# Kernel tuning notes

Measured on AMD Instinct MI355X. Metric: run time of the kernel, lower is better.

## Reference

```python
import jax, jax.numpy as jnp
import numpy as np

N, E, NF, EF, F = 50000, 100000, 20000, 40000, 10000
CIN, C, ED, S, H, L = 128, 128, 16, 8, 8, 3
EPS = 1e-5


def setup_inputs() -> dict:
    key = jax.random.key(0)
    ks = jax.random.split(key, 20)
    p = lambda k, shp: jax.random.normal(k, shp, dtype=jnp.float32) * 0.05
    return {
        "x": jax.random.normal(ks[0], (N, CIN), dtype=jnp.float32),
        "edge_attr": jax.random.normal(ks[1], (E, ED), dtype=jnp.float32),
        "frag_x": jax.random.normal(ks[2], (NF, CIN), dtype=jnp.float32),
        "frag_edge_attr": jax.random.normal(ks[3], (EF, ED), dtype=jnp.float32),
        "la_w": p(ks[4], (CIN, C)), "la_b": jnp.zeros((C,), jnp.float32),
        "lb_w": p(ks[5], (ED, C)), "lb_b": jnp.zeros((C,), jnp.float32),
        "bn1_g": jnp.ones((C,), jnp.float32), "bn1_b": jnp.zeros((C,), jnp.float32),
        "bn2_g": jnp.ones((C,), jnp.float32), "bn2_b": jnp.zeros((C,), jnp.float32),
        "wn": p(ks[6], (L, C, C)),
        "wb": p(ks[7], (L, S, C, C)),
        "wl": p(ks[8], (L, 3 * C, S)),
        "wlb": jnp.zeros((L, S), jnp.float32),
        "gate_w": p(ks[9], (3 * C, C)), "gate_b": jnp.zeros((C,), jnp.float32),
        "gat_wsrc": p(ks[10], (C, H * C)), "gat_wdst": p(ks[11], (C, H * C)),
        "gat_asrc": p(ks[12], (H, C)), "gat_adst": p(ks[13], (H, C)),
        "gat_bias": jnp.zeros((C,), jnp.float32),
        "out_w": p(ks[14], (2 * C, 1)), "out_b": jnp.zeros((1,), jnp.float32),
        "edge_index": jax.random.randint(ks[15], (2, E), 0, N),
        "frag_edge_index": jax.random.randint(ks[16], (2, EF), 0, NF),
        # sorted, covers every cluster id in [0, F) (each appears NF//F times)
        "cluster_index": (jnp.arange(NF) * F) // NF,
        "num_clusters": F,
    }


def reference(x, edge_attr, frag_x, frag_edge_attr, la_w, la_b, lb_w, lb_b,
              bn1_g, bn1_b, bn2_g, bn2_b, wn, wb, wl, wlb, gate_w, gate_b,
              gat_wsrc, gat_wdst, gat_asrc, gat_adst, gat_bias, out_w, out_b,
              edge_index, frag_edge_index, cluster_index, num_clusters):
    def bn(z, g, b):  # training-mode batch norm (biased var)
        mu = jnp.mean(z, 0)
        var = jnp.mean((z - mu) ** 2, 0)
        return (z - mu) * jax.lax.rsqrt(var + EPS) * g + b

    def ntn(h, ei, ea, Wn, Wb, Wl, bl):
        n = h.shape[0]
        xp = h @ Wn            # [n, C] node projection
        ep = ea @ Wn           # [e, C] (module reuses weight_node for edges)
        src, dst = ei[0], ei[1]
        xi, xj = xp[dst], xp[src]                       # per-edge gathers
        score = jnp.einsum('ec,scd,ed->es', xi, Wb, xj)  # bilinear score [e,S]
        block = jnp.concatenate([xi, ep, xj], axis=1) @ Wl + bl  # [e,S]
        alpha = jnp.tanh(score + block)
        e = xi.shape[0]
        msg = (jnp.maximum(xj, ep).reshape(e, S, C // S) * alpha[:, :, None]).reshape(e, C)
        return jax.ops.segment_sum(msg, dst, num_segments=n)  # aggr='add'

    def stack(h, ei, ea):
        for l in range(L):
            hh = jax.nn.relu(ntn(h, ei, ea, wn[l], wb[l], wl[l], wlb[l]))
            beta = jax.nn.relu(jnp.concatenate([h, hh, h - hh], axis=1) @ gate_w + gate_b)
            h = beta * h + (1.0 - beta) * hh
        return h

    # atom path
    x1 = jax.nn.relu(bn(x @ la_w + la_b, bn1_g, bn1_b))
    ea1 = jax.nn.relu(bn(edge_attr @ lb_w + lb_b, bn2_g, bn2_b))
    x1 = stack(x1, edge_index, ea1)
    mol_vec = jax.nn.relu(x1)  # global_add_pool with batch=arange(N) is identity

    # fragment path
    fx = jax.nn.relu(frag_x @ la_w + la_b)
    fea = jax.nn.relu(bn(frag_edge_attr @ lb_w + lb_b, bn2_g, bn2_b))
    fx = stack(fx, frag_edge_index, fea)
    frag_pool = jax.nn.relu(jax.ops.segment_sum(fx, cluster_index, num_segments=num_clusters))
    # consecutive_cluster perm = first occurrence of each cluster id (cluster_index sorted)
    perm = jnp.searchsorted(cluster_index, jnp.arange(num_clusters))

    # GATConv cross-attention, bipartite (frag_pool -> mol_vec), heads averaged
    n = mol_vec.shape[0]
    h_src = (frag_pool @ gat_wsrc).reshape(num_clusters, H, C)
    h_dst = (mol_vec @ gat_wdst).reshape(n, H, C)
    a_src = jnp.sum(h_src * gat_asrc, -1)   # [F,H]
    a_dst = jnp.sum(h_dst * gat_adst, -1)   # [n,H]
    el = jax.nn.leaky_relu(a_src + a_dst[perm], 0.01)
    m = jax.ops.segment_max(el, perm, num_segments=n)
    ex = jnp.exp(el - m[perm])
    sden = jax.ops.segment_sum(ex, perm, num_segments=n)
    att = ex / sden[perm]
    agg = jax.ops.segment_sum(h_src * att[:, :, None], perm, num_segments=n)
    frag_m_vec = jax.nn.relu(jnp.mean(agg, 1) + gat_bias)

    return jnp.concatenate([mol_vec, frag_m_vec], axis=1) @ out_w + out_b
```

## Files before the change

kernel.cpp:

```cpp
#include <hip/hip_runtime.h>
#include <hip/hip_bf16.h>
#include <hip/hip_fp8.h>

#define EPS 1e-5f

typedef short bf16x8 __attribute__((ext_vector_type(8)));
typedef short short4v __attribute__((ext_vector_type(4)));
typedef short short16v __attribute__((ext_vector_type(16)));
typedef float f32x4 __attribute__((ext_vector_type(4)));
typedef float f32x2 __attribute__((ext_vector_type(2)));
typedef unsigned char uchar16v __attribute__((ext_vector_type(16)));

static __device__ __forceinline__ short f2bf(float x) {
    __hip_bfloat16 h = __float2bfloat16(x);
    return *reinterpret_cast<short*>(&h);
}
static __device__ __forceinline__ float bf2f(short x) {
    __hip_bfloat16 h;
    *reinterpret_cast<short*>(&h) = x;
    return __bfloat162float(h);
}
static __device__ __forceinline__ unsigned char f2fp8(float x) {
    __hip_fp8_e4m3 q(x);
    return (unsigned char)q.__x;
}
static __device__ __forceinline__ float fp82f(unsigned char b) {
    __hip_fp8_e4m3 q;
    q.__x = (__hip_fp8_storage_t)b;
    return (float)q;
}
static __device__ __forceinline__ unsigned pack4_fp8(float v0, float v1, float v2, float v3) {
#if __has_builtin(__builtin_amdgcn_cvt_pk_fp8_f32)
    int pk = __builtin_amdgcn_cvt_pk_fp8_f32(v0, v1, 0, false);
    pk = __builtin_amdgcn_cvt_pk_fp8_f32(v2, v3, pk, true);
    return (unsigned)pk;
#else
    return (unsigned)f2fp8(v0) | ((unsigned)f2fp8(v1) << 8) |
           ((unsigned)f2fp8(v2) << 16) | ((unsigned)f2fp8(v3) << 24);
#endif
}
template<bool HI>
static __device__ __forceinline__ f32x2 unpack2_fp8(int w) {
#if __has_builtin(__builtin_amdgcn_cvt_pk_f32_fp8)
    return __builtin_amdgcn_cvt_pk_f32_fp8(w, HI);
#else
    f32x2 r;
    const int sh = HI ? 16 : 0;
    r[0] = fp82f((unsigned char)((w >> sh) & 0xff));
    r[1] = fp82f((unsigned char)((w >> (sh + 8)) & 0xff));
    return r;
#endif
}

template<int SPLIT, int ACT, int OUTM>
__global__ __launch_bounds__(256) void gemm_split(const float* __restrict__ A,
                                                  const short* __restrict__ BTh,
                                                  const short* __restrict__ BTl,
                                                  const float* __restrict__ bias,
                                                  void* __restrict__ Cout,
                                                  void* __restrict__ Cout2,
                                                  int M, int N, int K) {
    __shared__ short Ah[128][40];
    __shared__ short Al[128][40];
    __shared__ short Bh[128][40];
    __shared__ short Bl[128][40];
    const int tid = threadIdx.x;
    const int row0 = blockIdx.y * 128, col0 = blockIdx.x * 128;
    const int lane = tid & 63, w = tid >> 6;
    const int wr = w >> 1, wc = w & 1;
    const int lr = lane & 15, lg = lane >> 4;
    f32x4 acc[4][4] = {};

    for (int k0 = 0; k0 < K; k0 += 32) {
        #pragma unroll
        for (int i = 0; i < 4; ++i) {
            int idx = i * 256 + tid;
            int r = idx >> 3, q = idx & 7;
            int gr = row0 + r, gk = k0 + q * 4;
            f32x4 v;
            if (gr < M && gk + 3 < K) {
                v = *reinterpret_cast<const f32x4*>(&A[(size_t)gr * K + gk]);
            } else {
                #pragma unroll
                for (int j = 0; j < 4; ++j)
                    v[j] = (gr < M && gk + j < K) ? A[(size_t)gr * K + gk + j] : 0.f;
            }
            short4v h, l;
            #pragma unroll
            for (int j = 0; j < 4; ++j) {
                h[j] = f2bf(v[j]);
                l[j] = f2bf(v[j] - bf2f(h[j]));
            }
            *reinterpret_cast<short4v*>(&Ah[r][q * 4]) = h;
            *reinterpret_cast<short4v*>(&Al[r][q * 4]) = l;
        }
        #pragma unroll
        for (int i = 0; i < 4; ++i) {
            int idx = i * 256 + tid;
            int r = idx >> 3, q = idx & 7;
            int gc = col0 + r, gk = k0 + q * 4;
            short4v u, ul;
            if (gk + 3 < K) {
                u = *reinterpret_cast<const short4v*>(&BTh[(size_t)gc * K + gk]);
                if (SPLIT == 3) ul = *reinterpret_cast<const short4v*>(&BTl[(size_t)gc * K + gk]);
            } else {
                #pragma unroll
                for (int j = 0; j < 4; ++j) {
                    u[j] = (gk + j < K) ? BTh[(size_t)gc * K + gk + j] : (short)0;
                    if (SPLIT == 3) ul[j] = (gk + j < K) ? BTl[(size_t)gc * K + gk + j] : (short)0;
                }
            }
            *reinterpret_cast<short4v*>(&Bh[r][q * 4]) = u;
            if (SPLIT == 3) *reinterpret_cast<short4v*>(&Bl[r][q * 4]) = ul;
        }
        __syncthreads();
        bf16x8 afh[4], afl[4], bfh[4];
        #pragma unroll
        for (int mi = 0; mi < 4; ++mi) {
            afh[mi] = *reinterpret_cast<const bf16x8*>(&Ah[wr * 64 + mi * 16 + lr][lg * 8]);
            afl[mi] = *reinterpret_cast<const bf16x8*>(&Al[wr * 64 + mi * 16 + lr][lg * 8]);
        }
        #pragma unroll
        for (int ni = 0; ni < 4; ++ni)
            bfh[ni] = *reinterpret_cast<const bf16x8*>(&Bh[wc * 64 + ni * 16 + lr][lg * 8]);
        #pragma unroll
        for (int mi = 0; mi < 4; ++mi)
            #pragma unroll
            for (int ni = 0; ni < 4; ++ni) {
                acc[mi][ni] = __builtin_amdgcn_mfma_f32_16x16x32_bf16(afh[mi], bfh[ni], acc[mi][ni], 0, 0, 0);
                acc[mi][ni] = __builtin_amdgcn_mfma_f32_16x16x32_bf16(afl[mi], bfh[ni], acc[mi][ni], 0, 0, 0);
            }
        if (SPLIT == 3) {
            bf16x8 bfl[4];
            #pragma unroll
            for (int ni = 0; ni < 4; ++ni)
                bfl[ni] = *reinterpret_cast<const bf16x8*>(&Bl[wc * 64 + ni * 16 + lr][lg * 8]);
            #pragma unroll
            for (int mi = 0; mi < 4; ++mi)
                #pragma unroll
                for (int ni = 0; ni < 4; ++ni)
                    acc[mi][ni] = __builtin_amdgcn_mfma_f32_16x16x32_bf16(afh[mi], bfl[ni], acc[mi][ni], 0, 0, 0);
        }
        __syncthreads();
    }

    #pragma unroll
    for (int mi = 0; mi < 4; ++mi) {
        #pragma unroll
        for (int ni = 0; ni < 4; ++ni) {
            int col = col0 + wc * 64 + ni * 16 + lr;
            float bv = bias ? bias[col] : 0.f;
            #pragma unroll
            for (int r = 0; r < 4; ++r) {
                int row = row0 + wr * 64 + mi * 16 + lg * 4 + r;
                if (row >= M) continue;
                float v = acc[mi][ni][r] + bv;
                if (ACT) v = fmaxf(v, 0.f);
                if (OUTM == 0) ((float*)Cout)[(size_t)row * N + col] = v;
                else ((short*)Cout)[(size_t)row * N + col] = f2bf(v);
            }
        }
    }
}

__global__ __launch_bounds__(256) void ep_gemm64(const short* __restrict__ A,
                                                 const short* __restrict__ BT,
                                                 short* __restrict__ Cout, int M) {
    __shared__ short Bf[128 * 136];
    __shared__ short As[64 * 40];
    const int tid = threadIdx.x;
    const int row0 = blockIdx.x * 64;
    const int lane = tid & 63, w = tid >> 6;
    const int lr = lane & 15, lg = lane >> 4;

    #pragma unroll
    for (int i = 0; i < 8; ++i) {
        int idx = i * 256 + tid;
        int r = idx >> 4, q = idx & 15;
        *reinterpret_cast<bf16x8*>(&Bf[r * 136 + q * 8]) =
            *reinterpret_cast<const bf16x8*>(&BT[(size_t)r * 128 + q * 8]);
    }
    __syncthreads();

    f32x4 acc[4][2] = {};
    for (int k0 = 0; k0 < 128; k0 += 32) {
        #pragma unroll
        for (int i = 0; i < 2; ++i) {
            int idx = i * 256 + tid;
            int r = idx >> 3, q = idx & 7;
            int gr = row0 + r;
            short4v v;
            if (gr < M) {
                v = *reinterpret_cast<const short4v*>(&A[(size_t)gr * 128 + k0 + q * 4]);
            } else {
                #pragma unroll
                for (int j = 0; j < 4; ++j) v[j] = 0;
            }
            *reinterpret_cast<short4v*>(&As[r * 40 + q * 4]) = v;
        }
        __syncthreads();
        bf16x8 af[4], bfr[2];
        #pragma unroll
        for (int mi = 0; mi < 4; ++mi)
            af[mi] = *reinterpret_cast<const bf16x8*>(&As[(mi * 16 + lr) * 40 + lg * 8]);
        #pragma unroll
        for (int ni = 0; ni < 2; ++ni)
            bfr[ni] = *reinterpret_cast<const bf16x8*>(&Bf[(w * 32 + ni * 16 + lr) * 136 + k0 + lg * 8]);
        #pragma unroll
        for (int mi = 0; mi < 4; ++mi)
            #pragma unroll
            for (int ni = 0; ni < 2; ++ni)
                acc[mi][ni] = __builtin_amdgcn_mfma_f32_16x16x32_bf16(af[mi], bfr[ni], acc[mi][ni], 0, 0, 0);
        __syncthreads();
    }

    #pragma unroll
    for (int mi = 0; mi < 4; ++mi) {
        #pragma unroll
        for (int ni = 0; ni < 2; ++ni) {
            int col = w * 32 + ni * 16 + lr;
            #pragma unroll
            for (int r = 0; r < 4; ++r) {
                int row = row0 + mi * 16 + lg * 4 + r;
                if (row >= M) continue;
                Cout[(size_t)row * 128 + col] = f2bf(acc[mi][ni][r]);
            }
        }
    }
}

__global__ __launch_bounds__(256) void fused_xpy(const float* __restrict__ h,
                                                 const short* __restrict__ wnTh,
                                                 const short* __restrict__ wnTl,
                                                 const short* __restrict__ wbBT,
                                                 const float* __restrict__ wl1,
                                                 const float* __restrict__ wl2,
                                                 const float* __restrict__ wlb,
                                                 float* __restrict__ xpf,
                                                 float* __restrict__ ubuf,
                                                 unsigned char* __restrict__ Y, int M) {
    __shared__ short sbuf[15360];
    __shared__ unsigned char yb[64 * 136];
    short* Ah = sbuf;
    short* Al = sbuf + 2560;
    short* Bh = sbuf + 5120;
    short* Bl = sbuf + 10240;
    short* xpH = sbuf;

    const int tid = threadIdx.x;
    const int row0 = blockIdx.x * 64;
    const int lane = tid & 63, w = tid >> 6;
    const int lr = lane & 15, lg = lane >> 4;

    f32x4 acc1[4][2] = {};
    for (int k0 = 0; k0 < 128; k0 += 32) {
        #pragma unroll
        for (int i = 0; i < 2; ++i) {
            int idx = i * 256 + tid;
            int r = idx >> 3, q = idx & 7;
            int gr = row0 + r, gk = k0 + q * 4;
            f32x4 v;
            if (gr < M) {
                v = *reinterpret_cast<const f32x4*>(&h[(size_t)gr * 128 + gk]);
            } else {
                #pragma unroll
                for (int j = 0; j < 4; ++j) v[j] = 0.f;
            }
            short4v hh, ll;
            #pragma unroll
            for (int j = 0; j < 4; ++j) {
                hh[j] = f2bf(v[j]);
                ll[j] = f2bf(v[j] - bf2f(hh[j]));
            }
            *reinterpret_cast<short4v*>(&Ah[r * 40 + q * 4]) = hh;
            *reinterpret_cast<short4v*>(&Al[r * 40 + q * 4]) = ll;
        }
        #pragma unroll
        for (int i = 0; i < 4; ++i) {
            int idx = i * 256 + tid;
            int r = idx >> 3, q = idx & 7;
            int gk = k0 + q * 4;
            short4v bh = *reinterpret_cast<const short4v*>(&wnTh[(size_t)r * 128 + gk]);
            short4v bl = *reinterpret_cast<const short4v*>(&wnTl[(size_t)r * 128 + gk]);
            *reinterpret_cast<short4v*>(&Bh[r * 40 + q * 4]) = bh;
            *reinterpret_cast<short4v*>(&Bl[r * 40 + q * 4]) = bl;
        }
        __syncthreads();
        bf16x8 afh[4], afl[4], bfh[2], bfl[2];
        #pragma unroll
        for (int mi = 0; mi < 4; ++mi) {
            afh[mi] = *reinterpret_cast<const bf16x8*>(&Ah[(mi * 16 + lr) * 40 + lg * 8]);
            afl[mi] = *reinterpret_cast<const bf16x8*>(&Al[(mi * 16 + lr) * 40 + lg * 8]);
        }
        #pragma unroll
        for (int ni = 0; ni < 2; ++ni) {
            bfh[ni] = *reinterpret_cast<const bf16x8*>(&Bh[(w * 32 + ni * 16 + lr) * 40 + lg * 8]);
            bfl[ni] = *reinterpret_cast<const bf16x8*>(&Bl[(w * 32 + ni * 16 + lr) * 40 + lg * 8]);
        }
        #pragma unroll
        for (int mi = 0; mi < 4; ++mi)
            #pragma unroll
            for (int ni = 0; ni < 2; ++ni) {
                acc1[mi][ni] = __builtin_amdgcn_mfma_f32_16x16x32_bf16(afh[mi], bfh[ni], acc1[mi][ni], 0, 0, 0);
                acc1[mi][ni] = __builtin_amdgcn_mfma_f32_16x16x32_bf16(afl[mi], bfh[ni], acc1[mi][ni], 0, 0, 0);
                acc1[mi][ni] = __builtin_amdgcn_mfma_f32_16x16x32_bf16(afh[mi], bfl[ni], acc1[mi][ni], 0, 0, 0);
            }
        __syncthreads();
    }

    #pragma unroll
    for (int mi = 0; mi < 4; ++mi) {
        #pragma unroll
        for (int ni = 0; ni < 2; ++ni) {
            int col = w * 32 + ni * 16 + lr;
            #pragma unroll
            for (int r = 0; r < 4; ++r) {
                int rl = mi * 16 + lg * 4 + r;
                float v = acc1[mi][ni][r];
                xpH[rl * 136 + col] = f2bf(v);
                int row = row0 + rl;
                if (row < M) xpf[(size_t)row * 128 + col] = v;
            }
        }
    }
    __syncthreads();

    #pragma unroll
    for (int o = tid; o < 512; o += 256) {
        int rl = o >> 3, s = o & 7;
        int row = row0 + rl;
        if (row < M) {
            float p = wlb[s];
            #pragma unroll
            for (int j = 0; j < 16; ++j) {
                bf16x8 xv = *reinterpret_cast<const bf16x8*>(&xpH[rl * 136 + j * 8]);
                #pragma unroll
                for (int k = 0; k < 8; ++k)
                    p += bf2f(xv[k]) * wl2[(j * 8 + k) * 8 + s];
            }
            ubuf[(size_t)row * 8 + s] = p;
        }
    }

    for (int ct = 0; ct < 8; ++ct) {
        f32x4 accT[2][4] = {};
        #pragma unroll
        for (int k = 0; k < 4; ++k) {
            bf16x8 bfr[2];
            #pragma unroll
            for (int ni = 0; ni < 2; ++ni) {
                int col = ct * 128 + w * 32 + ni * 16 + lr;
                bfr[ni] = *reinterpret_cast<const bf16x8*>(&wbBT[(size_t)col * 128 + k * 32 + lg * 8]);
            }
            bf16x8 ah[4];
            #pragma unroll
            for (int mi = 0; mi < 4; ++mi)
                ah[mi] = *reinterpret_cast<const bf16x8*>(&xpH[(mi * 16 + lr) * 136 + k * 32 + lg * 8]);
            #pragma unroll
            for (int ni = 0; ni < 2; ++ni)
                #pragma unroll
                for (int mi = 0; mi < 4; ++mi)
                    accT[ni][mi] = __builtin_amdgcn_mfma_f32_16x16x32_bf16(bfr[ni], ah[mi], accT[ni][mi], 0, 0, 0);
        }
        #pragma unroll
        for (int ni = 0; ni < 2; ++ni) {
            int colg = w * 32 + ni * 16 + lg * 4;
            #pragma unroll
            for (int mi = 0; mi < 4; ++mi) {
                unsigned pk = pack4_fp8(accT[ni][mi][0] + wl1[(colg + 0) * 8 + ct],
                                        accT[ni][mi][1] + wl1[(colg + 1) * 8 + ct],
                                        accT[ni][mi][2] + wl1[(colg + 2) * 8 + ct],
                                        accT[ni][mi][3] + wl1[(colg + 3) * 8 + ct]);
                *reinterpret_cast<unsigned*>(&yb[(mi * 16 + lr) * 136 + colg]) = pk;
            }
        }
        __syncthreads();
        #pragma unroll
        for (int pass = 0; pass < 2; ++pass) {
            int flat = pass * 4096 + tid * 16;
            int rl = flat >> 7, cs = flat & 127;
            int row = row0 + rl;
            if (row < M) {
                uchar16v vv = *reinterpret_cast<const uchar16v*>(&yb[rl * 136 + cs]);
                *reinterpret_cast<uchar16v*>(&Y[(size_t)row * 1024 + ct * 128 + cs]) = vv;
            }
        }
        __syncthreads();
    }
}

__global__ __launch_bounds__(256) void edge_fused2(const float* __restrict__ xpf,
                                                   const short* __restrict__ ep,
                                                   const unsigned char* __restrict__ Y,
                                                   const int* __restrict__ ei,
                                                   const float* __restrict__ u,
                                                   const float* __restrict__ wl2g,
                                                   float* __restrict__ agg, int E) {
    __shared__ float swl[128][9];
    for (int i = threadIdx.x; i < 1024; i += 256) swl[i >> 3][i & 7] = wl2g[i];
    __syncthreads();
    int e = blockIdx.x * 4 + (threadIdx.x >> 6);
    if (e >= E) return;
    int l = threadIdx.x & 63;
    int s = l & 7, c0 = (l >> 3) * 16;
    int src = ei[e], dst = ei[E + e];
    const unsigned char* y = Y + (size_t)src * 1024 + s * 128 + c0;
    uchar16v yv = *reinterpret_cast<const uchar16v*>(y);
    const int* yw = reinterpret_cast<const int*>(&yv);
    float yf[16];
    #pragma unroll
    for (int q = 0; q < 4; ++q) {
        f32x2 a = unpack2_fp8<false>(yw[q]);
        f32x2 b = unpack2_fp8<true>(yw[q]);
        yf[q * 4 + 0] = a[0]; yf[q * 4 + 1] = a[1];
        yf[q * 4 + 2] = b[0]; yf[q * 4 + 3] = b[1];
    }
    const float* xi = xpf + (size_t)dst * 128 + c0;
    f32x4 xa = *reinterpret_cast<const f32x4*>(xi);
    f32x4 xb = *reinterpret_cast<const f32x4*>(xi + 4);
    f32x4 xc = *reinterpret_cast<const f32x4*>(xi + 8);
    f32x4 xd = *reinterpret_cast<const f32x4*>(xi + 12);
    short16v ev = *reinterpret_cast<const short16v*>(ep + (size_t)e * 128 + c0);
    float p = 0.f;
    #pragma unroll
    for (int j = 0; j < 4; ++j) {
        p += xa[j] * yf[j];
        p += xb[j] * yf[4 + j];
        p += xc[j] * yf[8 + j];
        p += xd[j] * yf[12 + j];
    }
    #pragma unroll
    for (int j = 0; j < 8; ++j) {
        p += bf2f(ev[j]) * swl[c0 + j][s];
        p += bf2f(ev[8 + j]) * swl[c0 + 8 + j][s];
    }
    p += __shfl_xor(p, 8); p += __shfl_xor(p, 16); p += __shfl_xor(p, 32);
    float alpha = tanhf(p + u[(size_t)src * 8 + s]);
    float aa0 = __shfl(alpha, l >> 4);
    float aa1 = __shfl(alpha, 4 + (l >> 4));
    float xj0 = xpf[(size_t)src * 128 + l];
    float xj1 = xpf[(size_t)src * 128 + l + 64];
    float e0 = bf2f(ep[(size_t)e * 128 + l]);
    float e1 = bf2f(ep[(size_t)e * 128 + l + 64]);
    atomicAdd(&agg[(size_t)dst * 128 + l],      fmaxf(xj0, e0) * aa0);
    atomicAdd(&agg[(size_t)dst * 128 + l + 64], fmaxf(xj1, e1) * aa1);
}

__global__ __launch_bounds__(256) void gate_gemm_split(float* __restrict__ h,
                                                       const float* __restrict__ aggv,
                                                       const short* __restrict__ BTh,
                                                       const short* __restrict__ BTl,
                                                       const float* __restrict__ gb,
                                                       int M) {
    __shared__ short Ah[64][40];
    __shared__ short Al[64][40];
    __shared__ short Bh[128][40];
    __shared__ short Bl[128][40];
    const int tid = threadIdx.x;
    const int row0 = blockIdx.x * 64;
    const int lane = tid & 63, w = tid >> 6;
    const int lr = lane & 15, lg = lane >> 4;
    f32x4 acc[4][2] = {};

    for (int k0 = 0; k0 < 256; k0 += 32) {
        int sec = k0 >> 7;
        #pragma unroll
        for (int i = 0; i < 2; ++i) {
            int idx = i * 256 + tid;
            int r = idx >> 3, q = idx & 7;
            int gr = row0 + r;
            int ks = (k0 & 127) + q * 4;
            f32x4 v;
            if (gr < M) {
                if (sec == 0) {
                    v = *reinterpret_cast<const f32x4*>(&h[(size_t)gr * 128 + ks]);
                } else {
                    f32x4 a = *reinterpret_cast<const f32x4*>(&aggv[(size_t)gr * 128 + ks]);
                    #pragma unroll
                    for (int j = 0; j < 4; ++j) v[j] = fmaxf(a[j], 0.f);
                }
            } else {
                #pragma unroll
                for (int j = 0; j < 4; ++j) v[j] = 0.f;
            }
            short4v hh, ll;
            #pragma unroll
            for (int j = 0; j < 4; ++j) {
                hh[j] = f2bf(v[j]);
                ll[j] = f2bf(v[j] - bf2f(hh[j]));
            }
            *reinterpret_cast<short4v*>(&Ah[r][q * 4]) = hh;
            *reinterpret_cast<short4v*>(&Al[r][q * 4]) = ll;
        }
        #pragma unroll
        for (int i = 0; i < 4; ++i) {
            int idx = i * 256 + tid;
            int r = idx >> 3, q = idx & 7;
            short4v uu = *reinterpret_cast<const short4v*>(&BTh[(size_t)r * 256 + k0 + q * 4]);
            short4v ul = *reinterpret_cast<const short4v*>(&BTl[(size_t)r * 256 + k0 + q * 4]);
            *reinterpret_cast<short4v*>(&Bh[r][q * 4]) = uu;
            *reinterpret_cast<short4v*>(&Bl[r][q * 4]) = ul;
        }
        __syncthreads();
        bf16x8 afh[4], afl[4], bfh[2], bfl[2];
        #pragma unroll
        for (int mi = 0; mi < 4; ++mi) {
            afh[mi] = *reinterpret_cast<const bf16x8*>(&Ah[mi * 16 + lr][lg * 8]);
            afl[mi] = *reinterpret_cast<const bf16x8*>(&Al[mi * 16 + lr][lg * 8]);
        }
        #pragma unroll
        for (int ni = 0; ni < 2; ++ni) {
            bfh[ni] = *reinterpret_cast<const bf16x8*>(&Bh[w * 32 + ni * 16 + lr][lg * 8]);
            bfl[ni] = *reinterpret_cast<const bf16x8*>(&Bl[w * 32 + ni * 16 + lr][lg * 8]);
        }
        #pragma unroll
        for (int mi = 0; mi < 4; ++mi)
            #pragma unroll
            for (int ni = 0; ni < 2; ++ni) {
                acc[mi][ni] = __builtin_amdgcn_mfma_f32_16x16x32_bf16(afh[mi], bfh[ni], acc[mi][ni], 0, 0, 0);
                acc[mi][ni] = __builtin_amdgcn_mfma_f32_16x16x32_bf16(afl[mi], bfh[ni], acc[mi][ni], 0, 0, 0);
                acc[mi][ni] = __builtin_amdgcn_mfma_f32_16x16x32_bf16(afh[mi], bfl[ni], acc[mi][ni], 0, 0, 0);
            }
        __syncthreads();
    }

    #pragma unroll
    for (int mi = 0; mi < 4; ++mi) {
        #pragma unroll
        for (int ni = 0; ni < 2; ++ni) {
            int col = w * 32 + ni * 16 + lr;
            float gbv = gb[col];
            #pragma unroll
            for (int r = 0; r < 4; ++r) {
                int row = row0 + mi * 16 + lg * 4 + r;
                if (row >= M) continue;
                float beta = fmaxf(acc[mi][ni][r] + gbv, 0.f);
                float hv = h[(size_t)row * 128 + col];
                float hh = fmaxf(aggv[(size_t)row * 128 + col], 0.f);
                h[(size_t)row * 128 + col] = beta * hv + (1.f - beta) * hh;
            }
        }
    }
}

__global__ void bn_stats(const float* __restrict__ z, float* __restrict__ gsum,
                         float* __restrict__ gsq, int M) {
    int c = threadIdx.x & 127;
    int rr = threadIdx.x >> 7;
    float s = 0.f, q = 0.f;
    for (int r = blockIdx.x * 2 + rr; r < M; r += gridDim.x * 2) {
        float v = z[(size_t)r * 128 + c];
        s += v; q += v * v;
    }
    __shared__ float ls[256], lq[256];
    ls[threadIdx.x] = s; lq[threadIdx.x] = q;
    __syncthreads();
    if (threadIdx.x < 128) {
        atomicAdd(&gsum[c], ls[threadIdx.x] + ls[threadIdx.x + 128]);
        atomicAdd(&gsq[c],  lq[threadIdx.x] + lq[threadIdx.x + 128]);
    }
}

__global__ void bn_apply(float* __restrict__ z, const float* __restrict__ gsum,
                         const float* __restrict__ gsq, const float* __restrict__ g,
                         const float* __restrict__ b, int M) {
    size_t total = (size_t)M * 128;
    for (size_t idx = (size_t)blockIdx.x * 256 + threadIdx.x; idx < total;
         idx += (size_t)gridDim.x * 256) {
        int c = idx & 127;
        float mu = gsum[c] / (float)M;
        float var = gsq[c] / (float)M - mu * mu;
        float rs = rsqrtf(var + EPS);
        float v = (z[idx] - mu) * rs * g[c] + b[c];
        z[idx] = fmaxf(v, 0.f);
    }
}

__global__ void bn_stats_bf(const short* __restrict__ z, float* __restrict__ gsum,
                            float* __restrict__ gsq, int M) {
    int c = threadIdx.x & 127;
    int rr = threadIdx.x >> 7;
    float s = 0.f, q = 0.f;
    for (int r = blockIdx.x * 2 + rr; r < M; r += gridDim.x * 2) {
        float v = bf2f(z[(size_t)r * 128 + c]);
        s += v; q += v * v;
    }
    __shared__ float ls[256], lq[256];
    ls[threadIdx.x] = s; lq[threadIdx.x] = q;
    __syncthreads();
    if (threadIdx.x < 128) {
        atomicAdd(&gsum[c], ls[threadIdx.x] + ls[threadIdx.x + 128]);
        atomicAdd(&gsq[c],  lq[threadIdx.x] + lq[threadIdx.x + 128]);
    }
}

__global__ void bn_apply_bf(short* __restrict__ z, const float* __restrict__ gsum,
                            const float* __restrict__ gsq, const float* __restrict__ g,
                            const float* __restrict__ b, int M) {
    size_t total = (size_t)M * 128;
    for (size_t idx = (size_t)blockIdx.x * 256 + threadIdx.x; idx < total;
         idx += (size_t)gridDim.x * 256) {
        int c = idx & 127;
        float mu = gsum[c] / (float)M;
        float var = gsq[c] / (float)M - mu * mu;
        float rs = rsqrtf(var + EPS);
        float v = (bf2f(z[idx]) - mu) * rs * g[c] + b[c];
        z[idx] = f2bf(fmaxf(v, 0.f));
    }
}

__global__ void transpose_split(const float* __restrict__ in, short* __restrict__ outh,
                                short* __restrict__ outl, int K, int N) {
    int idx = blockIdx.x * 256 + threadIdx.x;
    if (idx >= K * N) return;
    int nI = idx / K, k = idx - nI * K;
    float v = in[(size_t)k * N + nI];
    short h = f2bf(v);
    outh[idx] = h;
    outl[idx] = f2bf(v - bf2f(h));
}

__global__ void cvt_f2b(const float* __restrict__ in, short* __restrict__ out, int n) {
    int i = blockIdx.x * 256 + threadIdx.x;
    if (i < n) out[i] = f2bf(in[i]);
}

__global__ void gate_combine_split(const float* __restrict__ gw, short* __restrict__ BTh,
                                   short* __restrict__ BTl) {
    int idx = blockIdx.x * 256 + threadIdx.x;
    if (idx >= 128 * 256) return;
    int n = idx >> 8, k = idx & 255;
    float v;
    if (k < 128) v = gw[(size_t)k * 128 + n] + gw[(size_t)(256 + k) * 128 + n];
    else {
        int kk = k - 128;
        v = gw[(size_t)(128 + kk) * 128 + n] - gw[(size_t)(256 + kk) * 128 + n];
    }
    short h = f2bf(v);
    BTh[idx] = h;
    BTl[idx] = f2bf(v - bf2f(h));
}

__global__ void build_wm(const float* __restrict__ wsrc, float* __restrict__ wm) {
    int idx = blockIdx.x * 256 + threadIdx.x;
    if (idx >= 128 * 128) return;
    int d = idx >> 7, c = idx & 127;
    float s = 0.f;
    #pragma unroll
    for (int h = 0; h < 8; ++h) s += wsrc[(size_t)d * 1024 + h * 128 + c];
    wm[idx] = s * 0.125f;
}

__global__ void perm_build(const int* __restrict__ ci, int* __restrict__ perm, int NF) {
    int i = blockIdx.x * 256 + threadIdx.x;
    if (i >= NF) return;
    int c = ci[i];
    if (i == 0 || ci[i - 1] != c) perm[c] = i;
}

__global__ void seg_pool(const float* __restrict__ fx, const int* __restrict__ perm,
                         float* __restrict__ pool, int F, int NF) {
    int idx = blockIdx.x * 256 + threadIdx.x;
    if (idx >= F * 128) return;
    int f = idx >> 7, c = idx & 127;
    int s = perm[f];
    int e = (f + 1 < F) ? perm[f + 1] : NF;
    float acc = 0.f;
    for (int i = s; i < e; ++i) acc += fx[(size_t)i * 128 + c];
    pool[idx] = fmaxf(acc, 0.f);
}

__global__ __launch_bounds__(256) void out_phase1(const float* __restrict__ h,
                                                  const float* __restrict__ out_w,
                                                  const float* __restrict__ out_b,
                                                  const float* __restrict__ gat_bias,
                                                  float* __restrict__ out, int M) {
    int n = blockIdx.x * 4 + (threadIdx.x >> 6);
    if (n >= M) return;
    int l = threadIdx.x & 63;
    float p = fmaxf(h[(size_t)n * 128 + l], 0.f) * out_w[l]
            + fmaxf(h[(size_t)n * 128 + l + 64], 0.f) * out_w[l + 64];
    p += fmaxf(gat_bias[l], 0.f) * out_w[128 + l]
       + fmaxf(gat_bias[l + 64], 0.f) * out_w[128 + l + 64];
    #pragma unroll
    for (int off = 32; off; off >>= 1) p += __shfl_xor(p, off);
    if (l == 0) out[n] = p + out_b[0];
}

__global__ __launch_bounds__(256) void out_phase2(const float* __restrict__ fmv,
                                                  const int* __restrict__ perm,
                                                  const float* __restrict__ out_w,
                                                  const float* __restrict__ gat_bias,
                                                  float* __restrict__ out, int F) {
    int f = blockIdx.x * 4 + (threadIdx.x >> 6);
    if (f >= F) return;
    int l = threadIdx.x & 63;
    float p = fmv[(size_t)f * 128 + l] * out_w[128 + l]
            + fmv[(size_t)f * 128 + l + 64] * out_w[128 + l + 64];
    float b = fmaxf(gat_bias[l], 0.f) * out_w[128 + l]
            + fmaxf(gat_bias[l + 64], 0.f) * out_w[128 + l + 64];
    float d = p - b;
    #pragma unroll
    for (int off = 32; off; off >>= 1) d += __shfl_xor(d, off);
    if (l == 0) out[perm[f]] += d;
}

extern "C" void kernel_launch(void* const* d_in, const int* in_sizes, int n_in,
                              void* d_out, int out_size, void* d_ws, size_t ws_size,
                              hipStream_t stream) {
    const int N = 50000, E = 100000, NF = 20000, EF = 40000, F = 10000;

    const float* x          = (const float*)d_in[0];
    const float* edge_attr  = (const float*)d_in[1];
    const float* frag_x     = (const float*)d_in[2];
    const float* frag_ea    = (const float*)d_in[3];
    const float* la_w = (const float*)d_in[4];
    const float* la_b = (const float*)d_in[5];
    const float* lb_w = (const float*)d_in[6];
    const float* lb_b = (const float*)d_in[7];
    const float* bn1_g = (const float*)d_in[8];
    const float* bn1_b = (const float*)d_in[9];
    const float* bn2_g = (const float*)d_in[10];
    const float* bn2_b = (const float*)d_in[11];
    const float* wn = (const float*)d_in[12];
    const float* wb = (const float*)d_in[13];
    const float* wl = (const float*)d_in[14];
    const float* wlb = (const float*)d_in[15];
    const float* gate_w = (const float*)d_in[16];
    const float* gate_b = (const float*)d_in[17];
    const float* gat_wsrc = (const float*)d_in[18];
    const float* gat_bias = (const float*)d_in[22];
    const float* out_w = (const float*)d_in[23];
    const float* out_b = (const float*)d_in[24];
    const int* edge_index = (const int*)d_in[25];
    const int* frag_edge_index = (const int*)d_in[26];
    const int* cluster_index = (const int*)d_in[27];

    char* p = (char*)d_ws;
    auto alloc = [&](size_t bytes) { char* r = p; p += (bytes + 255) & ~(size_t)255; return (void*)r; };
    float* hA    = (float*)alloc((size_t)N * 128 * 4);
    short* ea1   = (short*)alloc((size_t)E * 128 * 2);
    float* xpf   = (float*)alloc((size_t)N * 128 * 4);
    short* ep    = (short*)alloc((size_t)E * 128 * 2);
    unsigned char* Y = (unsigned char*)alloc((size_t)N * 1024);
    float* agg   = (float*)alloc((size_t)N * 128 * 4);
    float* ubuf  = (float*)alloc((size_t)N * 8 * 4);
    short* la_wTh = (short*)alloc(128 * 128 * 2);
    short* la_wTl = (short*)alloc(128 * 128 * 2);
    short* lb_wTh = (short*)alloc(128 * 16 * 2);
    short* lb_wTl = (short*)alloc(128 * 16 * 2);
    short* wnTh   = (short*)alloc(3 * 128 * 128 * 2);
    short* wnTl   = (short*)alloc(3 * 128 * 128 * 2);
    short* wbH    = (short*)alloc(3 * 1024 * 128 * 2);
    short* gate2Th = (short*)alloc(128 * 256 * 2);
    short* gate2Tl = (short*)alloc(128 * 256 * 2);
    float* wmF    = (float*)alloc(128 * 128 * 4);
    short* wmTh   = (short*)alloc(128 * 128 * 2);
    short* wmTl   = (short*)alloc(128 * 128 * 2);
    float* stats  = (float*)alloc(256 * 4);
    char* yq = (char*)Y;
    float* fpool = (float*)yq;              yq += (size_t)F * 128 * 4;
    float* fmv   = (float*)yq;              yq += (size_t)F * 128 * 4;
    int*   perm  = (int*)yq;

    auto cdiv = [](int a, int b) { return (a + b - 1) / b; };

    transpose_split<<<cdiv(128 * 128, 256), 256, 0, stream>>>(la_w, la_wTh, la_wTl, 128, 128);
    transpose_split<<<cdiv(16 * 128, 256), 256, 0, stream>>>(lb_w, lb_wTh, lb_wTl, 16, 128);
    for (int l = 0; l < 3; ++l)
        transpose_split<<<cdiv(128 * 128, 256), 256, 0, stream>>>(
            wn + (size_t)l * 16384, wnTh + (size_t)l * 16384, wnTl + (size_t)l * 16384, 128, 128);
    cvt_f2b<<<cdiv(3 * 1024 * 128, 256), 256, 0, stream>>>(wb, wbH, 3 * 1024 * 128);
    gate_combine_split<<<cdiv(128 * 256, 256), 256, 0, stream>>>(gate_w, gate2Th, gate2Tl);
    build_wm<<<cdiv(128 * 128, 256), 256, 0, stream>>>(gat_wsrc, wmF);
    transpose_split<<<cdiv(128 * 128, 256), 256, 0, stream>>>(wmF, wmTh, wmTl, 128, 128);

    auto run_layer = [&](float* h, const short* ea_buf, const int* ei, int Mn, int Me, int layer) {
        const short* wnTh_l = wnTh + (size_t)layer * 16384;
        const short* wnTl_l = wnTl + (size_t)layer * 16384;
        const short* wb_l   = wbH + (size_t)layer * 131072;
        const float* wl_l   = wl + (size_t)layer * 384 * 8;
        const float* wlb_l  = wlb + (size_t)layer * 8;
        fused_xpy<<<cdiv(Mn, 64), 256, 0, stream>>>(h, wnTh_l, wnTl_l, wb_l, wl_l,
                                                    wl_l + 256 * 8, wlb_l, xpf, ubuf, Y, Mn);
        ep_gemm64<<<cdiv(Me, 64), 256, 0, stream>>>(ea_buf, wnTh_l, ep, Me);
        hipMemsetAsync(agg, 0, (size_t)Mn * 128 * 4, stream);
        edge_fused2<<<cdiv(Me, 4), 256, 0, stream>>>(xpf, ep, Y, ei, ubuf, wl_l + 128 * 8, agg, Me);
        gate_gemm_split<<<cdiv(Mn, 64), 256, 0, stream>>>(h, agg, gate2Th, gate2Tl, gate_b, Mn);
    };

    gemm_split<3, 0, 0><<<dim3(1, cdiv(N, 128)), 256, 0, stream>>>(x, la_wTh, la_wTl, la_b, hA, nullptr, N, 128, 128);
    hipMemsetAsync(stats, 0, 1024, stream);
    bn_stats<<<256, 256, 0, stream>>>(hA, stats, stats + 128, N);
    bn_apply<<<2048, 256, 0, stream>>>(hA, stats, stats + 128, bn1_g, bn1_b, N);

    gemm_split<3, 0, 1><<<dim3(1, cdiv(E, 128)), 256, 0, stream>>>(edge_attr, lb_wTh, lb_wTl, lb_b, ea1, nullptr, E, 128, 16);
    hipMemsetAsync(stats, 0, 1024, stream);
    bn_stats_bf<<<256, 256, 0, stream>>>(ea1, stats, stats + 128, E);
    bn_apply_bf<<<2048, 256, 0, stream>>>(ea1, stats, stats + 128, bn2_g, bn2_b, E);

    for (int l = 0; l < 3; ++l) run_layer(hA, ea1, edge_index, N, E, l);
    out_phase1<<<cdiv(N, 4), 256, 0, stream>>>(hA, out_w, out_b, gat_bias, (float*)d_out, N);

    gemm_split<3, 1, 0><<<dim3(1, cdiv(NF, 128)), 256, 0, stream>>>(frag_x, la_wTh, la_wTl, la_b, hA, nullptr, NF, 128, 128);

    gemm_split<3, 0, 1><<<dim3(1, cdiv(EF, 128)), 256, 0, stream>>>(frag_ea, lb_wTh, lb_wTl, lb_b, ea1, nullptr, EF, 128, 16);
    hipMemsetAsync(stats, 0, 1024, stream);
    bn_stats_bf<<<256, 256, 0, stream>>>(ea1, stats, stats + 128, EF);
    bn_apply_bf<<<2048, 256, 0, stream>>>(ea1, stats, stats + 128, bn2_g, bn2_b, EF);

    for (int l = 0; l < 3; ++l) run_layer(hA, ea1, frag_edge_index, NF, EF, l);

    perm_build<<<cdiv(NF, 256), 256, 0, stream>>>(cluster_index, perm, NF);
    seg_pool<<<cdiv(F * 128, 256), 256, 0, stream>>>(hA, perm, fpool, F, NF);
    gemm_split<3, 1, 0><<<dim3(1, cdiv(F, 128)), 256, 0, stream>>>(fpool, wmTh, wmTl, gat_bias, fmv, nullptr, F, 128, 128);
    out_phase2<<<cdiv(F, 4), 256, 0, stream>>>(fmv, perm, out_w, gat_bias, (float*)d_out, F);
}
```

Baseline: 1.082 ms.

## Fold agg zeroing into fused_xpy and process two edges per wave in edge kernel

Removes the per-layer hipMemsetAsync of the aggregation buffer by zeroing each block's rows of agg inside fused_xpy. The edge kernel now handles two edges per wavefront, issuing all gathers for both up front to raise memory-level parallelism and halving the grid size. This adds extra stores to fused_xpy and more registers in the edge kernel, which could lower occupancy.

```diff
diff --git a/kernel.cpp b/kernel.cpp
--- a/kernel.cpp
+++ b/kernel.cpp
@@ -238,7 +238,8 @@
                                                  const float* __restrict__ wlb,
                                                  float* __restrict__ xpf,
                                                  float* __restrict__ ubuf,
-                                                 unsigned char* __restrict__ Y, int M) {
+                                                 unsigned char* __restrict__ Y,
+                                                 float* __restrict__ agg, int M) {
     __shared__ short sbuf[15360];
     __shared__ unsigned char yb[64 * 136];
     short* Ah = sbuf;
@@ -251,6 +252,18 @@
     const int row0 = blockIdx.x * 64;
     const int lane = tid & 63, w = tid >> 6;
     const int lr = lane & 15, lg = lane >> 4;
+
+    {
+        f32x4 z = {0.f, 0.f, 0.f, 0.f};
+        #pragma unroll
+        for (int i = 0; i < 8; ++i) {
+            int flat = i * 1024 + tid * 4;
+            int rl = flat >> 7, cs = flat & 127;
+            int row = row0 + rl;
+            if (row < M)
+                *reinterpret_cast<f32x4*>(&agg[(size_t)row * 128 + cs]) = z;
+        }
+    }
 
     f32x4 acc1[4][2] = {};
     for (int k0 = 0; k0 < 128; k0 += 32) {
@@ -389,7 +402,7 @@
     }
 }
 
-__global__ __launch_bounds__(256) void edge_fused2(const float* __restrict__ xpf,
+__global__ __launch_bounds__(256) void edge_fused3(const float* __restrict__ xpf,
                                                    const short* __restrict__ ep,
                                                    const unsigned char* __restrict__ Y,
                                                    const int* __restrict__ ei,
@@ -399,51 +412,76 @@
     __shared__ float swl[128][9];
     for (int i = threadIdx.x; i < 1024; i += 256) swl[i >> 3][i & 7] = wl2g[i];
     __syncthreads();
-    int e = blockIdx.x * 4 + (threadIdx.x >> 6);
-    if (e >= E) return;
+    int w = threadIdx.x >> 6;
     int l = threadIdx.x & 63;
     int s = l & 7, c0 = (l >> 3) * 16;
-    int src = ei[e], dst = ei[E + e];
-    const unsigned char* y = Y + (size_t)src * 1024 + s * 128 + c0;
-    uchar16v yv = *reinterpret_cast<const uchar16v*>(y);
-    const int* yw = reinterpret_cast<const int*>(&yv);
-    float yf[16];
+    int e0 = blockIdx.x * 8 + w;
+    int e1 = e0 + 4;
+    bool ok0 = e0 < E, ok1 = e1 < E;
+    int src0 = ok0 ? ei[e0] : 0, dst0 = ok0 ? ei[E + e0] : 0;
+    int src1 = ok1 ? ei[e1] : 0, dst1 = ok1 ? ei[E + e1] : 0;
+
+    uchar16v yv0 = *reinterpret_cast<const uchar16v*>(Y + (size_t)src0 * 1024 + s * 128 + c0);
+    uchar16v yv1 = *reinterpret_cast<const uchar16v*>(Y + (size_t)src1 * 1024 + s * 128 + c0);
+    const float* xi0 = xpf + (size_t)dst0 * 128 + c0;
+    const float* xi1 = xpf + (size_t)dst1 * 128 + c0;
+    f32x4 xa0 = *reinterpret_cast<const f32x4*>(xi0);
+    f32x4 xb0 = *reinterpret_cast<const f32x4*>(xi0 + 4);
+    f32x4 xc0 = *reinterpret_cast<const f32x4*>(xi0 + 8);
+    f32x4 xd0 = *reinterpret_cast<const f32x4*>(xi0 + 12);
+    f32x4 xa1 = *reinterpret_cast<const f32x4*>(xi1);
+    f32x4 xb1 = *reinterpret_cast<const f32x4*>(xi1 + 4);
+    f32x4 xc1 = *reinterpret_cast<const f32x4*>(xi1 + 8);
+    f32x4 xd1 = *reinterpret_cast<const f32x4*>(xi1 + 12);
+    short16v ev0 = *reinterpret_cast<const short16v*>(ep + (size_t)e0 * 128 + c0);
+    short16v ev1 = *reinterpret_cast<const short16v*>(ep + (size_t)(ok1 ? e1 : e0) * 128 + c0);
+    float xj00 = xpf[(size_t)src0 * 128 + l];
+    float xj01 = xpf[(size_t)src0 * 128 + l + 64];
+    float xj10 = xpf[(size_t)src1 * 128 + l];
+    float xj11 = xpf[(size_t)src1 * 128 + l + 64];
+    float u0 = u[(size_t)src0 * 8 + s];
+    float u1 = u[(size_t)src1 * 8 + s];
+    float em00 = bf2f(ep[(size_t)e0 * 128 + l]);
+    float em01 = bf2f(ep[(size_t)e0 * 128 + l + 64]);
+    float em10 = bf2f(ep[(size_t)(ok1 ? e1 : e0) * 128 + l]);
+    float em11 = bf2f(ep[(size_t)(ok1 ? e1 : e0) * 128 + l + 64]);
+
+    const int* yw0 = reinterpret_cast<const int*>(&yv0);
+    const int* yw1 = reinterpret_cast<const int*>(&yv1);
+    float p0 = 0.f, p1 = 0.f;
     #pragma unroll
     for (int q = 0; q < 4; ++q) {
-        f32x2 a = unpack2_fp8<false>(yw[q]);
-        f32x2 b = unpack2_fp8<true>(yw[q]);
-        yf[q * 4 + 0] = a[0]; yf[q * 4 + 1] = a[1];
-        yf[q * 4 + 2] = b[0]; yf[q * 4 + 3] = b[1];
-    }
-    const float* xi = xpf + (size_t)dst * 128 + c0;
-    f32x4 xa = *reinterpret_cast<const f32x4*>(xi);
-    f32x4 xb = *reinterpret_cast<const f32x4*>(xi + 4);
-    f32x4 xc = *reinterpret_cast<const f32x4*>(xi + 8);
-    f32x4 xd = *reinterpret_cast<const f32x4*>(xi + 12);
-    short16v ev = *reinterpret_cast<const short16v*>(ep + (size_t)e * 128 + c0);
-    float p = 0.f;
-    #pragma unroll
-    for (int j = 0; j < 4; ++j) {
-        p += xa[j] * yf[j];
-        p += xb[j] * yf[4 + j];
-        p += xc[j] * yf[8 + j];
-        p += xd[j] * yf[12 + j];
+        f32x2 a0 = unpack2_fp8<false>(yw0[q]);
+        f32x2 b0 = unpack2_fp8<true>(yw0[q]);
+        f32x2 a1 = unpack2_fp8<false>(yw1[q]);
+        f32x2 b1 = unpack2_fp8<true>(yw1[q]);
+        const f32x4* xq0 = (q == 0) ? &xa0 : (q == 1) ? &xb0 : (q == 2) ? &xc0 : &xd0;
+        const f32x4* xq1 = (q == 0) ? &xa1 : (q == 1) ? &xb1 : (q == 2) ? &xc1 : &xd1;
+        p0 += (*xq0)[0] * a0[0] + (*xq0)[1] * a0[1] + (*xq0)[2] * b0[0] + (*xq0)[3] * b0[1];
+        p1 += (*xq1)[0] * a1[0] + (*xq1)[1] * a1[1] + (*xq1)[2] * b1[0] + (*xq1)[3] * b1[1];
     }
     #pragma unroll
     for (int j = 0; j < 8; ++j) {
-        p += bf2f(ev[j]) * swl[c0 + j][s];
-        p += bf2f(ev[8 + j]) * swl[c0 + 8 + j][s];
-    }
-    p += __shfl_xor(p, 8); p += __shfl_xor(p, 16); p += __shfl_xor(p, 32);
-    float alpha = tanhf(p + u[(size_t)src * 8 + s]);
-    float aa0 = __shfl(alpha, l >> 4);
-    float aa1 = __shfl(alpha, 4 + (l >> 4));
-    float xj0 = xpf[(size_t)src * 128 + l];
-    float xj1 = xpf[(size_t)src * 128 + l + 64];
-    float e0 = bf2f(ep[(size_t)e * 128 + l]);
-    float e1 = bf2f(ep[(size_t)e * 128 + l + 64]);
-    atomicAdd(&agg[(size_t)dst * 128 + l],      fmaxf(xj0, e0) * aa0);
-    atomicAdd(&agg[(size_t)dst * 128 + l + 64], fmaxf(xj1, e1) * aa1);
+        float w0 = swl[c0 + j][s], w1 = swl[c0 + 8 + j][s];
+        p0 += bf2f(ev0[j]) * w0 + bf2f(ev0[8 + j]) * w1;
+        p1 += bf2f(ev1[j]) * w0 + bf2f(ev1[8 + j]) * w1;
+    }
+    p0 += __shfl_xor(p0, 8); p0 += __shfl_xor(p0, 16); p0 += __shfl_xor(p0, 32);
+    p1 += __shfl_xor(p1, 8); p1 += __shfl_xor(p1, 16); p1 += __shfl_xor(p1, 32);
+    float alpha0 = tanhf(p0 + u0);
+    float alpha1 = tanhf(p1 + u1);
+    float a00 = __shfl(alpha0, l >> 4);
+    float a01 = __shfl(alpha0, 4 + (l >> 4));
+    float a10 = __shfl(alpha1, l >> 4);
+    float a11 = __shfl(alpha1, 4 + (l >> 4));
+    if (ok0) {
+        atomicAdd(&agg[(size_t)dst0 * 128 + l],      fmaxf(xj00, em00) * a00);
+        atomicAdd(&agg[(size_t)dst0 * 128 + l + 64], fmaxf(xj01, em01) * a01);
+    }
+    if (ok1) {
+        atomicAdd(&agg[(size_t)dst1 * 128 + l],      fmaxf(xj10, em10) * a10);
+        atomicAdd(&agg[(size_t)dst1 * 128 + l + 64], fmaxf(xj11, em11) * a11);
+    }
 }
 
 __global__ __launch_bounds__(256) void gate_gemm_split(float* __restrict__ h,
@@ -782,10 +820,9 @@
         const float* wl_l   = wl + (size_t)layer * 384 * 8;
         const float* wlb_l  = wlb + (size_t)layer * 8;
         fused_xpy<<<cdiv(Mn, 64), 256, 0, stream>>>(h, wnTh_l, wnTl_l, wb_l, wl_l,
-                                                    wl_l + 256 * 8, wlb_l, xpf, ubuf, Y, Mn);
+                                                    wl_l + 256 * 8, wlb_l, xpf, ubuf, Y, agg, Mn);
         ep_gemm64<<<cdiv(Me, 64), 256, 0, stream>>>(ea_buf, wnTh_l, ep, Me);
-        hipMemsetAsync(agg, 0, (size_t)Mn * 128 * 4, stream);
-        edge_fused2<<<cdiv(Me, 4), 256, 0, stream>>>(xpf, ep, Y, ei, ubuf, wl_l + 128 * 8, agg, Me);
+        edge_fused3<<<cdiv(Me, 8), 256, 0, stream>>>(xpf, ep, Y, ei, ubuf, wl_l + 128 * 8, agg, Me);
         gate_gemm_split<<<cdiv(Mn, 64), 256, 0, stream>>>(h, agg, gate2Th, gate2Tl, gate_b, Mn);
     };
 
```

Result: faster. 1.041 ms, median of 2 (-3.8%).
